# Optimization experiments

Hardware: AMD Instinct MI355X
Metric: run time of the kernel (lower is better)

Reference implementation:

```python
import jax, jax.numpy as jnp
import numpy as np

NEG_SLOPE = 0.2  # PyG GATConv default negative_slope


def gat_layer(x, src, dst, W, a_src, a_dst, bias, concat, N):
    """PyG GATConv: h = xW; e_ij = LeakyReLU(a_src.h_j + a_dst.h_i);
    alpha = segment-softmax over incoming edges of i; out_i = sum_j alpha_ij h_j."""
    H, C = a_src.shape
    h = (x @ W).reshape(N, H, C)                      # [N,H,C]
    alpha_s = jnp.einsum('nhc,hc->nh', h, a_src)      # [N,H]
    alpha_d = jnp.einsum('nhc,hc->nh', h, a_dst)      # [N,H]
    e = jax.nn.leaky_relu(alpha_s[src] + alpha_d[dst], NEG_SLOPE)  # [E,H]
    # numerically-stable segment softmax over destination nodes
    m = jax.ops.segment_max(e, dst, num_segments=N)   # [N,H]
    e = jnp.exp(e - m[dst])
    denom = jax.ops.segment_sum(e, dst, num_segments=N)
    alpha = e / (denom[dst] + 1e-16)                  # [E,H]
    msg = h[src] * alpha[:, :, None]                  # [E,H,C]
    out = jax.ops.segment_sum(msg, dst, num_segments=N)  # [N,H,C]
    out = out.reshape(N, H * C) if concat else out.mean(axis=1)
    return out + bias


def setup_inputs() -> dict:
    key = jax.random.key(0)
    ks = jax.random.split(key, 12)
    N, E, F_IN, C, H = 50000, 800000, 512, 32, 8
    s = 0.05
    x = jax.random.normal(ks[0], (N, F_IN), dtype=jnp.float32)
    edge_index = jax.random.randint(ks[1], (2, E), 0, N, dtype=jnp.int64)
    W1 = jax.random.normal(ks[2], (F_IN, H * C), dtype=jnp.float32) * s
    as1 = jax.random.normal(ks[3], (H, C), dtype=jnp.float32) * s
    ad1 = jax.random.normal(ks[4], (H, C), dtype=jnp.float32) * s
    b1 = jnp.zeros((H * C,), dtype=jnp.float32)
    W2 = jax.random.normal(ks[5], (H * C, H * C), dtype=jnp.float32) * s
    as2 = jax.random.normal(ks[6], (H, C), dtype=jnp.float32) * s
    ad2 = jax.random.normal(ks[7], (H, C), dtype=jnp.float32) * s
    b2 = jnp.zeros((C,), dtype=jnp.float32)
    Wp = jax.random.normal(ks[8], (C, 1), dtype=jnp.float32) * s
    bp = jnp.zeros((1,), dtype=jnp.float32)
    return {"edge_index": edge_index, "x": x, "W1": W1, "as1": as1, "ad1": ad1,
            "b1": b1, "W2": W2, "as2": as2, "ad2": ad2, "b2": b2,
            "Wp": Wp, "bp": bp}


def reference(edge_index, x, W1, as1, ad1, b1, W2, as2, ad2, b2, Wp, bp):
    N = x.shape[0]
    # PyG GATConv adds self-loops by default
    loops = jnp.arange(N, dtype=edge_index.dtype)
    src = jnp.concatenate([edge_index[0], loops])
    dst = jnp.concatenate([edge_index[1], loops])
    h = gat_layer(x, src, dst, W1, as1, ad1, b1, concat=True, N=N)
    h = jax.nn.relu(h)
    # F.dropout(training=self.training) is identity in eval mode
    h = gat_layer(h, src, dst, W2, as2, ad2, b2, concat=False, N=N)
    return jax.nn.sigmoid(h @ Wp + bp)   # [N,1]
```

## Files before the change

### kernel.cpp

```cpp
#include <hip/hip_runtime.h>
#include <math.h>

#define H_HEADS 8
#define C_DIM   32
#define HC      256
#define F_IN    512
#define NEG_SLOPE 0.2f

typedef __attribute__((ext_vector_type(8))) short    bf16x8;
typedef __attribute__((ext_vector_type(4))) short    s16x4;
typedef __attribute__((ext_vector_type(4))) float    f32x4;
typedef __attribute__((ext_vector_type(2))) float    f32x2;

__device__ __forceinline__ short f2bf(float f) {
    union { float f; unsigned u; } v; v.f = f;
    unsigned r = v.u + 0x7FFF + ((v.u >> 16) & 1);
    return (short)(r >> 16);
}

__device__ __forceinline__ bf16x8 cvt8(float4 a, float4 b) {
    union { bf16x8 v; unsigned u[4]; } r;
    asm("v_cvt_pk_bf16_f32 %0, %1, %2" : "=v"(r.u[0]) : "v"(a.x), "v"(a.y));
    asm("v_cvt_pk_bf16_f32 %0, %1, %2" : "=v"(r.u[1]) : "v"(a.z), "v"(a.w));
    asm("v_cvt_pk_bf16_f32 %0, %1, %2" : "=v"(r.u[2]) : "v"(b.x), "v"(b.y));
    asm("v_cvt_pk_bf16_f32 %0, %1, %2" : "=v"(r.u[3]) : "v"(b.z), "v"(b.w));
    return r.v;
}

__device__ __forceinline__ void gl2lds16(const short* g, short* l) {
    __builtin_amdgcn_global_load_lds(
        (const __attribute__((address_space(1))) void*)g,
        (__attribute__((address_space(3))) void*)l, 16, 0, 0);
}

__global__ void wfrag_kernel(const float* __restrict__ W1, const float* __restrict__ W2,
                             short* __restrict__ Wf1, short* __restrict__ Wf2)
{
    const int NW1 = F_IN * HC;
    const int NW2 = HC * HC;
    int tid = blockIdx.x * 256 + threadIdx.x;
    const float* W; short* Wf; int t;
    if (tid < NW1)            { W = W1; Wf = Wf1; t = tid; }
    else if (tid < NW1 + NW2) { W = W2; Wf = Wf2; t = tid - NW1; }
    else return;
    int j  = t & 7;
    int l  = (t >> 3) & 63;
    int nb = (t >> 9) & 15;
    int s  = t >> 13;
    int k  = s * 32 + (l >> 4) * 8 + j;
    int n  = nb * 16 + (l & 15);
    Wf[t] = f2bf(W[(size_t)k * HC + n]);
}

template<bool ABF16>
__global__ __launch_bounds__(256) void gemm_mfma(const void* __restrict__ Aptr,
    const short* __restrict__ Bf, unsigned char* __restrict__ h8,
    const float* __restrict__ a_s, const float* __restrict__ a_d,
    float* __restrict__ alpha_s, float* __restrict__ alpha_d, int M, int K)
{
    __shared__ short Bs[2][4096];
    __shared__ float Als[256], Ald[256];

    const int tid  = threadIdx.x;
    const int w    = tid >> 6;
    const int lane = tid & 63;
    const int quad = lane >> 4;
    const int ml   = lane & 15;
    const int cb   = blockIdx.x & 1;
    const int bm   = (blockIdx.x >> 1) * 64;

    const int rowA = bm + w * 16 + ml;
    const int rowL = rowA < M ? rowA : M - 1;

    f32x4 acc[8];
    #pragma unroll
    for (int nb = 0; nb < 8; ++nb) acc[nb] = (f32x4){0.f, 0.f, 0.f, 0.f};

    const float* A32 = (const float*)Aptr;
    const short* A16 = (const short*)Aptr;
    const int nsteps = K >> 5;

    {
        const short* g = Bf + (size_t)cb * 4096 + w * 512 + lane * 8;
        short* l = &Bs[0][w * 512 + lane * 8];
        gl2lds16(g, l);
        gl2lds16(g + 2048, l + 2048);
    }

    float4 p0, p1;
    bf16x8 pb;
    if (ABF16) {
        pb = *(const bf16x8*)(A16 + (size_t)rowL * K + quad * 8);
    } else {
        const float* ap = A32 + (size_t)rowL * K + quad * 8;
        p0 = *(const float4*)(ap);
        p1 = *(const float4*)(ap + 4);
    }

    for (int s = 0; s < nsteps; ++s) {
        __syncthreads();

        if (s + 1 < nsteps) {
            const short* g = Bf + (size_t)(s + 1) * 8192 + cb * 4096 + w * 512 + lane * 8;
            short* l = &Bs[(s + 1) & 1][w * 512 + lane * 8];
            gl2lds16(g, l);
            gl2lds16(g + 2048, l + 2048);
        }

        bf16x8 af;
        if (ABF16) {
            af = pb;
            if (s + 1 < nsteps)
                pb = *(const bf16x8*)(A16 + (size_t)rowL * K + (s + 1) * 32 + quad * 8);
        } else {
            af = cvt8(p0, p1);
            if (s + 1 < nsteps) {
                const float* ap = A32 + (size_t)rowL * K + (s + 1) * 32 + quad * 8;
                p0 = *(const float4*)(ap);
                p1 = *(const float4*)(ap + 4);
            }
        }

        const short* bsrc = &Bs[s & 1][lane * 8];
        #pragma unroll
        for (int nb = 0; nb < 8; ++nb) {
            bf16x8 bfr = *(const bf16x8*)(bsrc + nb * 512);
            acc[nb] = __builtin_amdgcn_mfma_f32_16x16x32_bf16(af, bfr, acc[nb], 0, 0, 0);
        }
    }

    float as_v[8], ad_v[8];
    #pragma unroll
    for (int nb = 0; nb < 8; ++nb) {
        as_v[nb] = a_s[cb * 128 + nb * 16 + ml];
        ad_v[nb] = a_d[cb * 128 + nb * 16 + ml];
    }

    #pragma unroll
    for (int r = 0; r < 4; ++r) {
        const int rl  = w * 16 + quad * 4 + r;
        const int row = bm + rl;

        if (row < M) {
            unsigned char* hrow = h8 + (size_t)row * HC + cb * 128;
            #pragma unroll
            for (int i = 0; i < 4; ++i) {
                int pk = __builtin_amdgcn_cvt_pk_fp8_f32(acc[2 * i][r], acc[2 * i + 1][r], 0, false);
                hrow[(2 * i) * 16 + ml]     = (unsigned char)(pk & 0xFF);
                hrow[(2 * i + 1) * 16 + ml] = (unsigned char)((pk >> 8) & 0xFF);
            }
        }

        float hs[4], hd[4];
        #pragma unroll
        for (int q = 0; q < 4; ++q) {
            hs[q] = acc[2 * q][r] * as_v[2 * q] + acc[2 * q + 1][r] * as_v[2 * q + 1];
            hd[q] = acc[2 * q][r] * ad_v[2 * q] + acc[2 * q + 1][r] * ad_v[2 * q + 1];
        }
        #pragma unroll
        for (int off = 1; off < 16; off <<= 1) {
            #pragma unroll
            for (int q = 0; q < 4; ++q) {
                hs[q] += __shfl_xor(hs[q], off);
                hd[q] += __shfl_xor(hd[q], off);
            }
        }
        if (ml == 0) {
            #pragma unroll
            for (int q = 0; q < 4; ++q) {
                Als[rl * 4 + q] = hs[q];
                Ald[rl * 4 + q] = hd[q];
            }
        }
    }
    __syncthreads();
    {
        int rl = tid >> 2, q = tid & 3;
        int row = bm + rl;
        if (row < M) {
            alpha_s[(size_t)row * H_HEADS + cb * 4 + q] = Als[tid];
            alpha_d[(size_t)row * H_HEADS + cb * 4 + q] = Ald[tid];
        }
    }
}

__global__ void zero_int(int* __restrict__ p, int n)
{
    int i = blockIdx.x * 256 + threadIdx.x;
    if (i < n) p[i] = 0;
}

__global__ void hist_kernel(const int* __restrict__ ei, int E, int N,
                            int* __restrict__ cnt)
{
    int e = blockIdx.x * 256 + threadIdx.x;
    if (e < E) atomicAdd(&cnt[ei[E + e]], 1);
    else if (e < E + N) atomicAdd(&cnt[e - E], 1);
}

__global__ __launch_bounds__(256) void scan_sum(const int* __restrict__ cnt, int n,
                                                int* __restrict__ chunk_sum)
{
    __shared__ int lds[256];
    int b = blockIdx.x, t = threadIdx.x;
    int base = b * 1024 + t * 4;
    int s = 0;
    #pragma unroll
    for (int j = 0; j < 4; ++j) { int i = base + j; if (i < n) s += cnt[i]; }
    lds[t] = s; __syncthreads();
    for (int off = 128; off > 0; off >>= 1) {
        if (t < off) lds[t] += lds[t + off];
        __syncthreads();
    }
    if (t == 0) chunk_sum[b] = lds[0];
}

__global__ __launch_bounds__(256) void scan_local(const int* __restrict__ cnt, int n,
    const int* __restrict__ chunk_sum, int nch, int* __restrict__ row_ptr)
{
    __shared__ int lds[256];
    int b = blockIdx.x, t = threadIdx.x;
    int lane = t & 63;

    int cs  = (lane < nch) ? chunk_sum[lane] : 0;
    int pre = (lane < b)   ? cs : 0;
    int tot = cs;
    #pragma unroll
    for (int off = 32; off > 0; off >>= 1) {
        pre += __shfl_xor(pre, off);
        tot += __shfl_xor(tot, off);
    }

    int base = b * 1024 + t * 4;
    int v[4]; int s = 0;
    #pragma unroll
    for (int j = 0; j < 4; ++j) { int i = base + j; v[j] = (i < n) ? cnt[i] : 0; s += v[j]; }
    lds[t] = s; __syncthreads();
    for (int off = 1; off < 256; off <<= 1) {
        int u = (t >= off) ? lds[t - off] : 0;
        __syncthreads();
        lds[t] += u;
        __syncthreads();
    }
    int run = lds[t] - s + pre;
    #pragma unroll
    for (int j = 0; j < 4; ++j) {
        int i = base + j;
        if (i < n) row_ptr[i] = run;
        run += v[j];
    }
    if (b == gridDim.x - 1 && t == 0) row_ptr[n] = tot;
}

__global__ void scatter_kernel(const int* __restrict__ ei, int E, int N,
    const int* __restrict__ row_ptr, int* __restrict__ cnt, int* __restrict__ es)
{
    int e = blockIdx.x * 256 + threadIdx.x;
    int src, dst;
    if (e < E)          { src = ei[e]; dst = ei[E + e]; }
    else if (e < E + N) { src = dst = e - E; }
    else return;
    int pos = row_ptr[dst] + atomicSub(&cnt[dst], 1) - 1;
    es[pos] = src;
}

#define ACC4(word, wgt, base_) do { \
    f32x2 lo_ = __builtin_amdgcn_cvt_pk_f32_fp8((word), false); \
    f32x2 hi_ = __builtin_amdgcn_cvt_pk_f32_fp8((word), true);  \
    acc[(base_) + 0] = fmaf((wgt), lo_[0], acc[(base_) + 0]); \
    acc[(base_) + 1] = fmaf((wgt), lo_[1], acc[(base_) + 1]); \
    acc[(base_) + 2] = fmaf((wgt), hi_[0], acc[(base_) + 2]); \
    acc[(base_) + 3] = fmaf((wgt), hi_[1], acc[(base_) + 3]); \
} while (0)

__device__ __forceinline__ float edge_w(float av, float ad8) {
    float e = av + ad8;
    return __expf(e > 0.f ? e : NEG_SLOPE * e);
}

__global__ __launch_bounds__(256) void agg1_kernel(const unsigned char* __restrict__ h8,
    const float* __restrict__ asb, const float* __restrict__ adb,
    const int* __restrict__ row_ptr, const int* __restrict__ es,
    const float* __restrict__ bias, short* __restrict__ z_bf, int N)
{
    const int l  = threadIdx.x & 63;
    const int i  = blockIdx.x * 4 + (threadIdx.x >> 6);
    if (i >= N) return;
    const int c  = l & 15;
    const int eo = l >> 4;
    const int hh = c >> 1;
    const float ad8 = adb[(size_t)i * 8 + hh];
    const int beg = row_ptr[i], end = row_ptr[i + 1];

    float acc[16];
    #pragma unroll
    for (int j = 0; j < 16; ++j) acc[j] = 0.f;
    float dsum = 0.f;

    int p = beg;
    for (; p + 7 < end; p += 8) {
        int s0 = es[p + eo], s1 = es[p + 4 + eo];
        float a0 = asb[(size_t)s0 * 8 + hh];
        float a1 = asb[(size_t)s1 * 8 + hh];
        uint4 h0 = *(const uint4*)(h8 + (size_t)s0 * 256 + c * 16);
        uint4 h1 = *(const uint4*)(h8 + (size_t)s1 * 256 + c * 16);
        float w0 = edge_w(a0, ad8);
        float w1 = edge_w(a1, ad8);
        ACC4(h0.x, w0, 0); ACC4(h0.y, w0, 4); ACC4(h0.z, w0, 8); ACC4(h0.w, w0, 12);
        ACC4(h1.x, w1, 0); ACC4(h1.y, w1, 4); ACC4(h1.z, w1, 8); ACC4(h1.w, w1, 12);
        dsum += w0 + w1;
    }
    for (; p < end; p += 4) {
        int pe = p + eo;
        int pc = pe < end ? pe : end - 1;
        int s0 = es[pc];
        float w0 = pe < end ? edge_w(asb[(size_t)s0 * 8 + hh], ad8) : 0.f;
        uint4 h0 = *(const uint4*)(h8 + (size_t)s0 * 256 + c * 16);
        ACC4(h0.x, w0, 0); ACC4(h0.y, w0, 4); ACC4(h0.z, w0, 8); ACC4(h0.w, w0, 12);
        dsum += w0;
    }

    #pragma unroll
    for (int j = 0; j < 16; ++j) {
        acc[j] += __shfl_xor(acc[j], 32);
        acc[j] += __shfl_xor(acc[j], 16);
    }
    dsum += __shfl_xor(dsum, 32);
    dsum += __shfl_xor(dsum, 16);

    float inv = 1.f / (dsum + 1e-16f);
    if (eo == 0) {
        union { short s[16]; bf16x8 v[2]; } zz;
        #pragma unroll
        for (int j = 0; j < 16; ++j) {
            float z = acc[j] * inv + bias[c * 16 + j];
            zz.s[j] = f2bf(z > 0.f ? z : 0.f);
        }
        *(bf16x8*)(z_bf + (size_t)i * HC + c * 16)     = zz.v[0];
        *(bf16x8*)(z_bf + (size_t)i * HC + c * 16 + 8) = zz.v[1];
    }
}

__global__ __launch_bounds__(256) void agg2_kernel(const unsigned char* __restrict__ h8,
    const float* __restrict__ asb, const float* __restrict__ adb,
    const int* __restrict__ row_ptr, const int* __restrict__ es,
    const float* __restrict__ b2, const float* __restrict__ Wp,
    const float* __restrict__ bp, float* __restrict__ out, int N)
{
    const int l  = threadIdx.x & 63;
    const int i  = blockIdx.x * 4 + (threadIdx.x >> 6);
    if (i >= N) return;
    const int c  = l & 15;
    const int eo = l >> 4;
    const int hh = c >> 1;
    const float ad8 = adb[(size_t)i * 8 + hh];
    const int beg = row_ptr[i], end = row_ptr[i + 1];

    float acc[16];
    #pragma unroll
    for (int j = 0; j < 16; ++j) acc[j] = 0.f;
    float dsum = 0.f;

    int p = beg;
    for (; p + 7 < end; p += 8) {
        int s0 = es[p + eo], s1 = es[p + 4 + eo];
        float a0 = asb[(size_t)s0 * 8 + hh];
        float a1 = asb[(size_t)s1 * 8 + hh];
        uint4 h0 = *(const uint4*)(h8 + (size_t)s0 * 256 + c * 16);
        uint4 h1 = *(const uint4*)(h8 + (size_t)s1 * 256 + c * 16);
        float w0 = edge_w(a0, ad8);
        float w1 = edge_w(a1, ad8);
        ACC4(h0.x, w0, 0); ACC4(h0.y, w0, 4); ACC4(h0.z, w0, 8); ACC4(h0.w, w0, 12);
        ACC4(h1.x, w1, 0); ACC4(h1.y, w1, 4); ACC4(h1.z, w1, 8); ACC4(h1.w, w1, 12);
        dsum += w0 + w1;
    }
    for (; p < end; p += 4) {
        int pe = p + eo;
        int pc = pe < end ? pe : end - 1;
        int s0 = es[pc];
        float w0 = pe < end ? edge_w(asb[(size_t)s0 * 8 + hh], ad8) : 0.f;
        uint4 h0 = *(const uint4*)(h8 + (size_t)s0 * 256 + c * 16);
        ACC4(h0.x, w0, 0); ACC4(h0.y, w0, 4); ACC4(h0.z, w0, 8); ACC4(h0.w, w0, 12);
        dsum += w0;
    }

    #pragma unroll
    for (int j = 0; j < 16; ++j) {
        acc[j] += __shfl_xor(acc[j], 32);
        acc[j] += __shfl_xor(acc[j], 16);
    }
    dsum += __shfl_xor(dsum, 32);
    dsum += __shfl_xor(dsum, 16);

    float inv = 1.f / (dsum + 1e-16f);
    const int wb = (c & 1) << 4;
    float partial = 0.f;
    #pragma unroll
    for (int j = 0; j < 16; ++j) partial = fmaf(acc[j] * inv, Wp[wb + j], partial);
    if (eo == 0 && c < 2) {
        #pragma unroll
        for (int j = 0; j < 16; ++j) partial += 8.f * b2[c * 16 + j] * Wp[c * 16 + j];
    }
    #pragma unroll
    for (int off = 8; off > 0; off >>= 1) partial += __shfl_xor(partial, off);
    if (l == 0) out[i] = 1.f / (1.f + __expf(-(0.125f * partial + bp[0])));
}

extern "C" void kernel_launch(void* const* d_in, const int* in_sizes, int n_in,
                              void* d_out, int out_size, void* d_ws, size_t ws_size,
                              hipStream_t stream)
{
    const int*   ei  = (const int*)d_in[0];
    const float* x   = (const float*)d_in[1];
    const float* W1  = (const float*)d_in[2];
    const float* as1 = (const float*)d_in[3];
    const float* ad1 = (const float*)d_in[4];
    const float* b1  = (const float*)d_in[5];
    const float* W2  = (const float*)d_in[6];
    const float* as2 = (const float*)d_in[7];
    const float* ad2 = (const float*)d_in[8];
    const float* b2  = (const float*)d_in[9];
    const float* Wp  = (const float*)d_in[10];
    const float* bp  = (const float*)d_in[11];
    float* out = (float*)d_out;

    const int E = in_sizes[0] / 2;
    const int N = in_sizes[1] / F_IN;
    const int ET = E + N;

    float*         asb = (float*)d_ws;
    float*         adb = asb + (size_t)N * H_HEADS;
    unsigned char* h8  = (unsigned char*)(adb + (size_t)N * H_HEADS);
    short*         z1b = (short*)(h8 + (size_t)N * HC);
    short*         Wf1 = z1b + (size_t)N * HC;
    short*         Wf2 = Wf1 + (size_t)F_IN * HC;
    int*           es  = (int*)(Wf2 + (size_t)HC * HC);
    int* cnt       = es + ET;
    int* row_ptr   = cnt + N;
    int* chunk_sum = row_ptr + N + 1;

    const int NCH = (N + 1023) / 1024;
    const int MB  = ((N + 63) / 64) * 2;
    const int NB4 = (N + 3) / 4;

    zero_int<<<(N + 255) / 256, 256, 0, stream>>>(cnt, N);
    hist_kernel<<<(ET + 255) / 256, 256, 0, stream>>>(ei, E, N, cnt);
    scan_sum<<<NCH, 256, 0, stream>>>(cnt, N, chunk_sum);
    scan_local<<<NCH, 256, 0, stream>>>(cnt, N, chunk_sum, NCH, row_ptr);
    scatter_kernel<<<(ET + 255) / 256, 256, 0, stream>>>(ei, E, N, row_ptr, cnt, es);

    wfrag_kernel<<<(F_IN * HC + HC * HC + 255) / 256, 256, 0, stream>>>(W1, W2, Wf1, Wf2);

    gemm_mfma<false><<<MB, 256, 0, stream>>>(x, Wf1, h8, as1, ad1, asb, adb, N, F_IN);
    agg1_kernel<<<NB4, 256, 0, stream>>>(h8, asb, adb, row_ptr, es, b1, z1b, N);

    gemm_mfma<true><<<MB, 256, 0, stream>>>(z1b, Wf2, h8, as2, ad2, asb, adb, N, HC);
    agg2_kernel<<<NB4, 256, 0, stream>>>(h8, asb, adb, row_ptr, es, b2, Wp, bp, out, N);
}
```

Measured before the change: 399.8 us.

## Process two K-steps per barrier in GEMM and fuse weight prep into scatter

```diff
diff --git a/kernel.cpp b/kernel.cpp
--- a/kernel.cpp
+++ b/kernel.cpp
@@ -33,24 +33,12 @@
         (__attribute__((address_space(3))) void*)l, 16, 0, 0);
 }
 
-__global__ void wfrag_kernel(const float* __restrict__ W1, const float* __restrict__ W2,
-                             short* __restrict__ Wf1, short* __restrict__ Wf2)
-{
-    const int NW1 = F_IN * HC;
-    const int NW2 = HC * HC;
-    int tid = blockIdx.x * 256 + threadIdx.x;
-    const float* W; short* Wf; int t;
-    if (tid < NW1)            { W = W1; Wf = Wf1; t = tid; }
-    else if (tid < NW1 + NW2) { W = W2; Wf = Wf2; t = tid - NW1; }
-    else return;
-    int j  = t & 7;
-    int l  = (t >> 3) & 63;
-    int nb = (t >> 9) & 15;
-    int s  = t >> 13;
-    int k  = s * 32 + (l >> 4) * 8 + j;
-    int n  = nb * 16 + (l & 15);
-    Wf[t] = f2bf(W[(size_t)k * HC + n]);
-}
+#define STAGE(ss, buf) do { \
+    const short* g_ = Bf + (size_t)(ss) * 8192 + cb * 4096 + w * 512 + lane * 8; \
+    short* l_ = &Bs[buf][((ss) & 1) * 4096 + w * 512 + lane * 8]; \
+    gl2lds16(g_, l_); \
+    gl2lds16(g_ + 2048, l_ + 2048); \
+} while (0)
 
 template<bool ABF16>
 __global__ __launch_bounds__(256) void gemm_mfma(const void* __restrict__ Aptr,
@@ -58,7 +46,7 @@
     const float* __restrict__ a_s, const float* __restrict__ a_d,
     float* __restrict__ alpha_s, float* __restrict__ alpha_d, int M, int K)
 {
-    __shared__ short Bs[2][4096];
+    __shared__ short Bs[2][8192];
     __shared__ float Als[256], Ald[256];
 
     const int tid  = threadIdx.x;
@@ -71,61 +59,68 @@
 
     const int rowA = bm + w * 16 + ml;
     const int rowL = rowA < M ? rowA : M - 1;
+    const size_t aoff = (size_t)rowL * K + quad * 8;
+    const float* Ar32 = (const float*)Aptr + aoff;
+    const short* Ar16 = (const short*)Aptr + aoff;
 
     f32x4 acc[8];
     #pragma unroll
     for (int nb = 0; nb < 8; ++nb) acc[nb] = (f32x4){0.f, 0.f, 0.f, 0.f};
 
-    const float* A32 = (const float*)Aptr;
-    const short* A16 = (const short*)Aptr;
-    const int nsteps = K >> 5;
-
-    {
-        const short* g = Bf + (size_t)cb * 4096 + w * 512 + lane * 8;
-        short* l = &Bs[0][w * 512 + lane * 8];
-        gl2lds16(g, l);
-        gl2lds16(g + 2048, l + 2048);
-    }
-
-    float4 p0, p1;
-    bf16x8 pb;
+    const int nph = K >> 6;
+
+    STAGE(0, 0);
+    STAGE(1, 0);
+
+    float4 pf0, pf1, pf2, pf3;
+    bf16x8 pb0, pb1;
     if (ABF16) {
-        pb = *(const bf16x8*)(A16 + (size_t)rowL * K + quad * 8);
+        pb0 = *(const bf16x8*)(Ar16);
+        pb1 = *(const bf16x8*)(Ar16 + 32);
     } else {
-        const float* ap = A32 + (size_t)rowL * K + quad * 8;
-        p0 = *(const float4*)(ap);
-        p1 = *(const float4*)(ap + 4);
-    }
-
-    for (int s = 0; s < nsteps; ++s) {
+        pf0 = *(const float4*)(Ar32);
+        pf1 = *(const float4*)(Ar32 + 4);
+        pf2 = *(const float4*)(Ar32 + 32);
+        pf3 = *(const float4*)(Ar32 + 36);
+    }
+
+    for (int p = 0; p < nph; ++p) {
         __syncthreads();
 
-        if (s + 1 < nsteps) {
-            const short* g = Bf + (size_t)(s + 1) * 8192 + cb * 4096 + w * 512 + lane * 8;
-            short* l = &Bs[(s + 1) & 1][w * 512 + lane * 8];
-            gl2lds16(g, l);
-            gl2lds16(g + 2048, l + 2048);
-        }
-
-        bf16x8 af;
+        if (p + 1 < nph) {
+            STAGE(2 * p + 2, (p + 1) & 1);
+            STAGE(2 * p + 3, (p + 1) & 1);
+        }
+
+        bf16x8 af0, af1;
         if (ABF16) {
-            af = pb;
-            if (s + 1 < nsteps)
-                pb = *(const bf16x8*)(A16 + (size_t)rowL * K + (s + 1) * 32 + quad * 8);
+            af0 = pb0; af1 = pb1;
+            if (p + 1 < nph) {
+                pb0 = *(const bf16x8*)(Ar16 + (p + 1) * 64);
+                pb1 = *(const bf16x8*)(Ar16 + (p + 1) * 64 + 32);
+            }
         } else {
-            af = cvt8(p0, p1);
-            if (s + 1 < nsteps) {
-                const float* ap = A32 + (size_t)rowL * K + (s + 1) * 32 + quad * 8;
-                p0 = *(const float4*)(ap);
-                p1 = *(const float4*)(ap + 4);
+            af0 = cvt8(pf0, pf1);
+            af1 = cvt8(pf2, pf3);
+            if (p + 1 < nph) {
+                pf0 = *(const float4*)(Ar32 + (p + 1) * 64);
+                pf1 = *(const float4*)(Ar32 + (p + 1) * 64 + 4);
+                pf2 = *(const float4*)(Ar32 + (p + 1) * 64 + 32);
+                pf3 = *(const float4*)(Ar32 + (p + 1) * 64 + 36);
             }
         }
 
-        const short* bsrc = &Bs[s & 1][lane * 8];
+        const short* b0 = &Bs[p & 1][lane * 8];
         #pragma unroll
         for (int nb = 0; nb < 8; ++nb) {
-            bf16x8 bfr = *(const bf16x8*)(bsrc + nb * 512);
-            acc[nb] = __builtin_amdgcn_mfma_f32_16x16x32_bf16(af, bfr, acc[nb], 0, 0, 0);
+            bf16x8 bfr = *(const bf16x8*)(b0 + nb * 512);
+            acc[nb] = __builtin_amdgcn_mfma_f32_16x16x32_bf16(af0, bfr, acc[nb], 0, 0, 0);
+        }
+        const short* b1 = &Bs[p & 1][4096 + lane * 8];
+        #pragma unroll
+        for (int nb = 0; nb < 8; ++nb) {
+            bf16x8 bfr = *(const bf16x8*)(b1 + nb * 512);
+            acc[nb] = __builtin_amdgcn_mfma_f32_16x16x32_bf16(af1, bfr, acc[nb], 0, 0, 0);
         }
     }
 
@@ -252,10 +247,28 @@
     if (b == gridDim.x - 1 && t == 0) row_ptr[n] = tot;
 }
 
-__global__ void scatter_kernel(const int* __restrict__ ei, int E, int N,
-    const int* __restrict__ row_ptr, int* __restrict__ cnt, int* __restrict__ es)
-{
+__global__ void scatter_wfrag_kernel(const int* __restrict__ ei, int E, int N,
+    const int* __restrict__ row_ptr, int* __restrict__ cnt, int* __restrict__ es,
+    const float* __restrict__ W1, const float* __restrict__ W2,
+    short* __restrict__ Wf1, short* __restrict__ Wf2)
+{
+    const int NW1 = F_IN * HC;
+    const int NW2 = HC * HC;
     int e = blockIdx.x * 256 + threadIdx.x;
+
+    if (e < NW1 + NW2) {
+        const float* W; short* Wf; int t;
+        if (e < NW1) { W = W1; Wf = Wf1; t = e; }
+        else         { W = W2; Wf = Wf2; t = e - NW1; }
+        int j  = t & 7;
+        int l  = (t >> 3) & 63;
+        int nb = (t >> 9) & 15;
+        int s  = t >> 13;
+        int k  = s * 32 + (l >> 4) * 8 + j;
+        int n  = nb * 16 + (l & 15);
+        Wf[t] = f2bf(W[(size_t)k * HC + n]);
+    }
+
     int src, dst;
     if (e < E)          { src = ei[e]; dst = ei[E + e]; }
     else if (e < E + N) { src = dst = e - E; }
@@ -447,9 +460,8 @@
     hist_kernel<<<(ET + 255) / 256, 256, 0, stream>>>(ei, E, N, cnt);
     scan_sum<<<NCH, 256, 0, stream>>>(cnt, N, chunk_sum);
     scan_local<<<NCH, 256, 0, stream>>>(cnt, N, chunk_sum, NCH, row_ptr);
-    scatter_kernel<<<(ET + 255) / 256, 256, 0, stream>>>(ei, E, N, row_ptr, cnt, es);
-
-    wfrag_kernel<<<(F_IN * HC + HC * HC + 255) / 256, 256, 0, stream>>>(W1, W2, Wf1, Wf2);
+    scatter_wfrag_kernel<<<(ET + 255) / 256, 256, 0, stream>>>(ei, E, N, row_ptr, cnt, es,
+                                                               W1, W2, Wf1, Wf2);
 
     gemm_mfma<false><<<MB, 256, 0, stream>>>(x, Wf1, h8, as1, ad1, asb, adb, N, F_IN);
     agg1_kernel<<<NB4, 256, 0, stream>>>(h8, asb, adb, row_ptr, es, b1, z1b, N);
```

Result: no change. 393.6 us (-1.5%).
